# Optimization experiments

Hardware: AMD Instinct MI355X
Metric: run time of the kernel (lower is better)

The kernel has to match this reference:

```python
import math
import jax, jax.numpy as jnp
import numpy as np

B, T, H, E, K, F = 4, 4096, 512, 8, 2, 2048
CAP_FACTOR, ROUND_TO = 0.3125, 128


def _capacity(num_tokens):
    cap = math.ceil(CAP_FACTOR * num_tokens)
    cap = ROUND_TO * math.ceil(cap / ROUND_TO)
    return max(1, min(cap, num_tokens))


def setup_inputs() -> dict:
    key = jax.random.key(0)
    k0, k1, k2, k3 = jax.random.split(key, 4)
    x = jax.random.normal(k0, (B, T, H), jnp.float32)
    router_w = jax.random.normal(k1, (H, E), jnp.float32) * 0.02
    w1 = jax.random.normal(k2, (E, H, F), jnp.float32) * (1.0 / np.sqrt(H))
    b1 = jnp.zeros((E, F), jnp.float32)
    w2 = jax.random.normal(k3, (E, F, H), jnp.float32) * (1.0 / np.sqrt(F))
    b2 = jnp.zeros((E, H), jnp.float32)
    return {"x": x, "router_w": router_w, "w1": w1, "b1": b1, "w2": w2, "b2": b2}


def reference(x, router_w, w1, b1, w2, b2):
    Bc, Tc, Hc = x.shape
    n = Bc * Tc
    cap = _capacity(n)  # static: 5120
    flat = x.reshape(n, Hc)

    # Router + top-k selection (fp32 logits, softmax over selected logits)
    logits = (flat @ router_w).astype(jnp.float32)          # [n, E]
    sel_logits, expert_idx = jax.lax.top_k(logits, K)       # [n, K]
    weights = jax.nn.softmax(sel_logits, axis=-1)           # [n, K]

    # Flatten (token, k) assignments and sort by expert (stable)
    fe = expert_idx.reshape(-1).astype(jnp.int32)           # [n*K]
    fw = weights.reshape(-1)
    tok = jnp.broadcast_to(jnp.arange(n, dtype=jnp.int32)[:, None], expert_idx.shape).reshape(-1)
    order = jnp.argsort(fe)  # jax sort is stable
    se, st, sw = fe[order], tok[order], fw[order]

    # Per-expert slot index; assignments beyond capacity are dropped
    counts = jnp.bincount(se, length=E)                     # [E]
    offsets = (jnp.cumsum(counts) - counts).astype(jnp.int32)
    slot = jnp.arange(se.shape[0], dtype=jnp.int32) - offsets[se]
    keep = slot < cap
    sw = jnp.where(keep, sw, 0.0)                           # dropped tokens contribute 0

    # Pack into fixed-capacity expert buffers (out-of-range slots dropped)
    sx = flat[st]                                           # [n*K, H]
    expert_inputs = jnp.zeros((E, cap, Hc), flat.dtype).at[se, slot].set(sx, mode='drop')

    # Grouped expert MLP: Dense(F) -> GELU -> Dense(H)
    h = jax.nn.gelu(jnp.einsum('ech,ehf->ecf', expert_inputs, w1) + b1[:, None, :])
    out = jnp.einsum('ecf,efh->ech', h, w2) + b2[:, None, :]

    # Zero invalid (unused) slots
    clipped = jnp.minimum(counts, cap)
    valid = (jnp.arange(cap, dtype=jnp.int32)[None, :] < clipped[:, None])[..., None]
    out = jnp.where(valid, out, 0)

    # Scatter-combine weighted expert outputs back to tokens
    slot_c = jnp.minimum(slot, cap - 1)                     # dropped rows have weight 0
    gathered = out[se, slot_c] * sw[:, None].astype(out.dtype)
    combined = jnp.zeros((n, Hc), out.dtype).at[st].add(gathered)
    return combined.reshape(Bc, Tc, Hc)
```

## Files before the change

kernel.cpp:

```cpp
#include <hip/hip_runtime.h>
#include <hip/hip_bf16.h>

#define NTOK 16384
#define HD   512
#define ED   8
#define FD   2048
#define CAP  5120
#define NA   32768

typedef __bf16 bf16x8 __attribute__((ext_vector_type(8)));
typedef float  f32x4  __attribute__((ext_vector_type(4)));

static constexpr size_t OFF_EIDX = 0;
static constexpr size_t OFF_WGT  = 131072;
static constexpr size_t OFF_STOK = 262144;
static constexpr size_t OFF_SWGT = 458752;
static constexpr size_t OFF_W2T  = 1u << 20;
static constexpr size_t OFF_H    = OFF_W2T + (size_t)ED*HD*FD*2;
static constexpr size_t OFF_W1T  = OFF_H   + (size_t)ED*CAP*FD*2;
static constexpr size_t OFF_XBF  = OFF_W1T + (size_t)ED*FD*HD*2;

__device__ __forceinline__ unsigned short f2bf(float f) {
    __bf16 b = (__bf16)f;
    return __builtin_bit_cast(unsigned short, b);
}

__device__ __forceinline__ float gelu_fast(float v) {
    const float u = 1.5957691216057308f * (v + 0.044715f * v * v * v);
    return v / (1.f + __expf(-u));
}

__global__ __launch_bounds__(256) void transpose_cast_kernel(
    const float* __restrict__ in, unsigned short* __restrict__ out, int R, int C)
{
    __shared__ unsigned short tile[32][33];
    const int e = blockIdx.z;
    in  += (size_t)e * R * C;
    out += (size_t)e * R * C;
    const int r0 = blockIdx.y * 32, c0 = blockIdx.x * 32;
    const int tr = threadIdx.x >> 3, tc = (threadIdx.x & 7) * 4;
    const float4 v = *(const float4*)(in + (size_t)(r0 + tr) * C + c0 + tc);
    tile[tr][tc + 0] = f2bf(v.x);
    tile[tr][tc + 1] = f2bf(v.y);
    tile[tr][tc + 2] = f2bf(v.z);
    tile[tr][tc + 3] = f2bf(v.w);
    __syncthreads();
    ushort4 o;
    o.x = tile[tc + 0][tr]; o.y = tile[tc + 1][tr];
    o.z = tile[tc + 2][tr]; o.w = tile[tc + 3][tr];
    *(ushort4*)(out + (size_t)(c0 + tr) * R + r0 + tc) = o;
}

__global__ __launch_bounds__(256) void router_kernel(
    const float* __restrict__ x, const float* __restrict__ rw,
    int* __restrict__ eidx, float* __restrict__ wgt,
    unsigned short* __restrict__ xbf)
{
    __shared__ float rws[HD * ED];
    const int tid = threadIdx.x;
    for (int i = tid * 4; i < HD * ED; i += 256 * 4)
        *(float4*)(rws + i) = *(const float4*)(rw + i);
    __syncthreads();

    const int wid = tid >> 6, lane = tid & 63;
    const int t = blockIdx.x * 4 + wid;
    const float* xr = x + (size_t)t * HD;

    float acc[ED];
#pragma unroll
    for (int e = 0; e < ED; e++) acc[e] = 0.f;

    float4 xv0 = *(const float4*)(xr + lane * 8);
    float4 xv1 = *(const float4*)(xr + lane * 8 + 4);
    float xv[8] = {xv0.x, xv0.y, xv0.z, xv0.w, xv1.x, xv1.y, xv1.z, xv1.w};

    union { unsigned short us[8]; uint4 v; } pk;
#pragma unroll
    for (int j = 0; j < 8; j++) pk.us[j] = f2bf(xv[j]);
    *(uint4*)(xbf + (size_t)t * HD + lane * 8) = pk.v;

#pragma unroll
    for (int j = 0; j < 8; j++) {
        const int h = lane * 8 + j;
#pragma unroll
        for (int e = 0; e < ED; e++) acc[e] += xv[j] * rws[h * ED + e];
    }
#pragma unroll
    for (int off = 32; off >= 1; off >>= 1) {
#pragma unroll
        for (int e = 0; e < ED; e++) acc[e] += __shfl_down(acc[e], off);
    }
    if (lane == 0) {
        int e0 = 0; float l0 = acc[0];
        for (int e = 1; e < ED; e++) if (acc[e] > l0) { l0 = acc[e]; e0 = e; }
        int e1 = 0; float l1 = -1e30f;
        for (int e = 0; e < ED; e++) {
            if (e == e0) continue;
            if (acc[e] > l1) { l1 = acc[e]; e1 = e; }
        }
        const float ex = expf(l1 - l0);
        const float inv = 1.f / (1.f + ex);
        eidx[t * 2 + 0] = e0;  eidx[t * 2 + 1] = e1;
        wgt [t * 2 + 0] = inv; wgt [t * 2 + 1] = ex * inv;
    }
}

__global__ __launch_bounds__(1024) void scan_kernel(
    const int* __restrict__ eidx, const float* __restrict__ wgt,
    int* __restrict__ stok, float* __restrict__ swgt)
{
    __shared__ int running[ED];
    __shared__ int wcnt[16][ED];
    const int tid = threadIdx.x;

    for (int i = tid; i < ED * CAP; i += 1024) stok[i] = -1;
    if (tid < ED) running[tid] = 0;
    __syncthreads();

    const int lane = tid & 63, wid = tid >> 6;
    const unsigned long long below = (1ull << lane) - 1ull;

    for (int c = 0; c < NA / 1024; c++) {
        const int a = c * 1024 + tid;
        const int e = eidx[a];
        const float w = wgt[a];
        int myrank = 0;
#pragma unroll
        for (int ee = 0; ee < ED; ee++) {
            unsigned long long m = __ballot(e == ee);
            if (ee == e) myrank = __popcll(m & below);
            if (lane == 0) wcnt[wid][ee] = __popcll(m);
        }
        __syncthreads();
        int woff = 0;
        for (int ww = 0; ww < wid; ww++) woff += wcnt[ww][e];
        const int slot = running[e] + woff + myrank;
        if (slot < CAP) {
            stok[e * CAP + slot] = a >> 1;
            swgt[e * CAP + slot] = w;
        }
        __syncthreads();
        if (tid < ED) {
            int tot = 0;
            for (int ww = 0; ww < 16; ww++) tot += wcnt[ww][tid];
            running[tid] += tot;
        }
        __syncthreads();
    }
}

template<int KD, int ND, int NT, bool FUSE>
__global__ __launch_bounds__(256) void gemm_mfma(
    const unsigned short* __restrict__ Abase,
    const unsigned short* __restrict__ Bt,
    const float* __restrict__ bias,
    const int* __restrict__ stok,
    const float* __restrict__ swgt,
    unsigned short* __restrict__ hout,
    float* __restrict__ out)
{
    constexpr int RS   = 40;
    constexpr int BUFE = 128 * RS;
    __shared__ __align__(16) unsigned short As[2 * BUFE];
    __shared__ __align__(16) unsigned short Bs[2 * BUFE];

    const int tid = threadIdx.x;
    const int e  = blockIdx.x & 7;
    const int g  = blockIdx.x >> 3;
    const int n0 = (g % NT) * 128;
    const int m0 = (g / NT) * 128;

    const int q  = tid & 3;
    const int r1 = tid >> 2;
    const int r2 = r1 + 64;

    size_t ai1, ai2;
    if (!FUSE) {
        const int t1 = stok[e * CAP + m0 + r1];
        const int t2 = stok[e * CAP + m0 + r2];
        ai1 = (size_t)(t1 >= 0 ? t1 : 0);
        ai2 = (size_t)(t2 >= 0 ? t2 : 0);
    } else {
        ai1 = (size_t)(e * CAP + m0 + r1);
        ai2 = (size_t)(e * CAP + m0 + r2);
    }
    const unsigned short* arow1 = Abase + ai1 * KD + q * 8;
    const unsigned short* arow2 = Abase + ai2 * KD + q * 8;
    const unsigned short* brow1 = Bt + ((size_t)e * ND + n0 + r1) * KD + q * 8;
    const unsigned short* brow2 = Bt + ((size_t)e * ND + n0 + r2) * KD + q * 8;

    const int oW1 = r1 * RS + q * 8;
    const int oW2 = r2 * RS + q * 8;

    const int lane = tid & 63;
    const int wid  = tid >> 6;
    const int wrow = (wid & 1) * 64;
    const int wcol = (wid >> 1) * 64;
    const int l15  = lane & 15;
    const int quad = lane >> 4;
    const int fA   = (wrow + l15) * RS + quad * 8;
    const int fB   = (wcol + l15) * RS + quad * 8;

    f32x4 acc[4][4];
#pragma unroll
    for (int i = 0; i < 4; i++)
#pragma unroll
        for (int j = 0; j < 4; j++) acc[i][j] = (f32x4)0.f;

    float4 ra1 = *(const float4*)(arow1);
    float4 ra2 = *(const float4*)(arow2);
    float4 rb1 = *(const float4*)(brow1);
    float4 rb2 = *(const float4*)(brow2);
    *(float4*)(&As[oW1]) = ra1;
    *(float4*)(&As[oW2]) = ra2;
    *(float4*)(&Bs[oW1]) = rb1;
    *(float4*)(&Bs[oW2]) = rb2;
    if (32 < KD) {
        ra1 = *(const float4*)(arow1 + 32);
        ra2 = *(const float4*)(arow2 + 32);
        rb1 = *(const float4*)(brow1 + 32);
        rb2 = *(const float4*)(brow2 + 32);
    }
    __syncthreads();

#define COMPUTE(PBUF)                                                          \
    {                                                                          \
        const unsigned short* Ab = As + (PBUF) * BUFE;                         \
        const unsigned short* Bb = Bs + (PBUF) * BUFE;                         \
        bf16x8 af[4], bfv[4];                                                  \
        _Pragma("unroll")                                                      \
        for (int i = 0; i < 4; i++) af[i]  = *(const bf16x8*)(Ab + fA + i * 16 * RS); \
        _Pragma("unroll")                                                      \
        for (int j = 0; j < 4; j++) bfv[j] = *(const bf16x8*)(Bb + fB + j * 16 * RS); \
        _Pragma("unroll")                                                      \
        for (int i = 0; i < 4; i++)                                            \
            _Pragma("unroll")                                                  \
            for (int j = 0; j < 4; j++)                                        \
                acc[i][j] = __builtin_amdgcn_mfma_f32_16x16x32_bf16(           \
                    af[i], bfv[j], acc[i][j], 0, 0, 0);                        \
    }

    int rbuf = 0;
    for (int kc = 0; kc < KD; kc += 32) {
        const int wb = (rbuf ^ 1) * BUFE;
        if (kc + 32 < KD) {
            *(float4*)(&As[wb + oW1]) = ra1;
            *(float4*)(&As[wb + oW2]) = ra2;
            *(float4*)(&Bs[wb + oW1]) = rb1;
            *(float4*)(&Bs[wb + oW2]) = rb2;
            if (kc + 64 < KD) {
                ra1 = *(const float4*)(arow1 + kc + 64);
                ra2 = *(const float4*)(arow2 + kc + 64);
                rb1 = *(const float4*)(brow1 + kc + 64);
                rb2 = *(const float4*)(brow2 + kc + 64);
            }
        }
        COMPUTE(rbuf);
        __syncthreads();
        rbuf ^= 1;
    }
#undef COMPUTE

    if (!FUSE) {
#pragma unroll
        for (int i = 0; i < 4; i++) {
#pragma unroll
            for (int g2 = 0; g2 < 4; g2++) {
                const int m = wrow + i * 16 + quad * 4 + g2;
                unsigned short* hrow = hout + ((size_t)e * CAP + m0 + m) * FD + n0;
#pragma unroll
                for (int j = 0; j < 4; j++) {
                    const int n = wcol + j * 16 + l15;
                    const float v = acc[i][j][g2] + bias[(size_t)e * ND + n0 + n];
                    hrow[n] = f2bf(gelu_fast(v));
                }
            }
        }
    } else {
#pragma unroll
        for (int i = 0; i < 4; i++) {
#pragma unroll
            for (int g2 = 0; g2 < 4; g2++) {
                const int m = wrow + i * 16 + quad * 4 + g2;
                const int tok = stok[e * CAP + m0 + m];
                if (tok >= 0) {
                    const float w = swgt[e * CAP + m0 + m];
                    float* orow = out + (size_t)tok * HD + n0;
#pragma unroll
                    for (int j = 0; j < 4; j++) {
                        const int n = wcol + j * 16 + l15;
                        const float v = (acc[i][j][g2] + bias[(size_t)e * ND + n0 + n]) * w;
                        atomicAdd(orow + n, v);
                    }
                }
            }
        }
    }
}

extern "C" void kernel_launch(void* const* d_in, const int* in_sizes, int n_in,
                              void* d_out, int out_size, void* d_ws, size_t ws_size,
                              hipStream_t stream)
{
    const float* x  = (const float*)d_in[0];
    const float* rw = (const float*)d_in[1];
    const float* w1 = (const float*)d_in[2];
    const float* b1 = (const float*)d_in[3];
    const float* w2 = (const float*)d_in[4];
    const float* b2 = (const float*)d_in[5];
    float* out = (float*)d_out;

    char* ws = (char*)d_ws;
    int*   eidx = (int*)  (ws + OFF_EIDX);
    float* wgt  = (float*)(ws + OFF_WGT);
    int*   stok = (int*)  (ws + OFF_STOK);
    float* swgt = (float*)(ws + OFF_SWGT);
    unsigned short* w2t  = (unsigned short*)(ws + OFF_W2T);
    unsigned short* hbuf = (unsigned short*)(ws + OFF_H);
    unsigned short* w1t  = (unsigned short*)(ws + OFF_W1T);
    unsigned short* xbf  = (unsigned short*)(ws + OFF_XBF);

    transpose_cast_kernel<<<dim3(FD / 32, HD / 32, ED), 256, 0, stream>>>(w1, w1t, HD, FD);
    transpose_cast_kernel<<<dim3(HD / 32, FD / 32, ED), 256, 0, stream>>>(w2, w2t, FD, HD);
    router_kernel<<<NTOK / 4, 256, 0, stream>>>(x, rw, eidx, wgt, xbf);
    scan_kernel<<<1, 1024, 0, stream>>>(eidx, wgt, stok, swgt);
    hipMemsetAsync(d_out, 0, (size_t)out_size * sizeof(float), stream);

    gemm_mfma<HD, FD, FD/128, false>
        <<<8 * (FD/128) * (CAP/128), 256, 0, stream>>>(
        xbf, w1t, b1, stok, nullptr, hbuf, nullptr);

    gemm_mfma<FD, HD, HD/128, true>
        <<<8 * (HD/128) * (CAP/128), 256, 0, stream>>>(
        hbuf, w2t, b2, stok, swgt, nullptr, out);
}
```

Baseline: 521.5 us.

## Restructure scan into two-pass prefix, fuse output zeroing, reorganize GEMM LDS layout

Three independent changes. The output zeroing moves from a separate memset into the router kernel. The single-block scan is rewritten to count all chunks first, build the per-warp offsets in one serial pass, then scatter without per-chunk barriers. The GEMM shared-memory tiles switch from a padded row-major layout (stride 40) to a k-quad-major layout of 16-byte vectors, so fragment loads index contiguous vectors, which changes the LDS bank access pattern.

```diff
diff --git a/kernel.cpp b/kernel.cpp
--- a/kernel.cpp
+++ b/kernel.cpp
@@ -54,7 +54,7 @@
 __global__ __launch_bounds__(256) void router_kernel(
     const float* __restrict__ x, const float* __restrict__ rw,
     int* __restrict__ eidx, float* __restrict__ wgt,
-    unsigned short* __restrict__ xbf)
+    unsigned short* __restrict__ xbf, float* __restrict__ outz)
 {
     __shared__ float rws[HD * ED];
     const int tid = threadIdx.x;
@@ -65,6 +65,10 @@
     const int wid = tid >> 6, lane = tid & 63;
     const int t = blockIdx.x * 4 + wid;
     const float* xr = x + (size_t)t * HD;
+
+    const float4 z = make_float4(0.f, 0.f, 0.f, 0.f);
+    *(float4*)(outz + (size_t)t * HD + lane * 8)     = z;
+    *(float4*)(outz + (size_t)t * HD + lane * 8 + 4) = z;
 
     float acc[ED];
 #pragma unroll
@@ -109,43 +113,48 @@
     const int* __restrict__ eidx, const float* __restrict__ wgt,
     int* __restrict__ stok, float* __restrict__ swgt)
 {
-    __shared__ int running[ED];
-    __shared__ int wcnt[16][ED];
+    __shared__ int wcnt[32][16][ED];
     const int tid = threadIdx.x;
-
-    for (int i = tid; i < ED * CAP; i += 1024) stok[i] = -1;
-    if (tid < ED) running[tid] = 0;
-    __syncthreads();
-
     const int lane = tid & 63, wid = tid >> 6;
     const unsigned long long below = (1ull << lane) - 1ull;
+
+    for (int i = tid; i < ED * CAP; i += 1024) stok[i] = -1;
+
+    for (int c = 0; c < NA / 1024; c++) {
+        const int e = eidx[c * 1024 + tid];
+#pragma unroll
+        for (int ee = 0; ee < ED; ee++) {
+            unsigned long long m = __ballot(e == ee);
+            if (lane == 0) wcnt[c][wid][ee] = __popcll(m);
+        }
+    }
+    __syncthreads();
+
+    if (tid < ED) {
+        int run = 0;
+        for (int c = 0; c < 32; c++)
+            for (int w = 0; w < 16; w++) {
+                const int v = wcnt[c][w][tid];
+                wcnt[c][w][tid] = run;
+                run += v;
+            }
+    }
+    __syncthreads();
 
     for (int c = 0; c < NA / 1024; c++) {
         const int a = c * 1024 + tid;
         const int e = eidx[a];
-        const float w = wgt[a];
         int myrank = 0;
 #pragma unroll
         for (int ee = 0; ee < ED; ee++) {
             unsigned long long m = __ballot(e == ee);
             if (ee == e) myrank = __popcll(m & below);
-            if (lane == 0) wcnt[wid][ee] = __popcll(m);
-        }
-        __syncthreads();
-        int woff = 0;
-        for (int ww = 0; ww < wid; ww++) woff += wcnt[ww][e];
-        const int slot = running[e] + woff + myrank;
+        }
+        const int slot = wcnt[c][wid][e] + myrank;
         if (slot < CAP) {
             stok[e * CAP + slot] = a >> 1;
-            swgt[e * CAP + slot] = w;
-        }
-        __syncthreads();
-        if (tid < ED) {
-            int tot = 0;
-            for (int ww = 0; ww < 16; ww++) tot += wcnt[ww][tid];
-            running[tid] += tot;
-        }
-        __syncthreads();
+            swgt[e * CAP + slot] = wgt[a];
+        }
     }
 }
 
@@ -159,8 +168,7 @@
     unsigned short* __restrict__ hout,
     float* __restrict__ out)
 {
-    constexpr int RS   = 40;
-    constexpr int BUFE = 128 * RS;
+    constexpr int BUFE = 4096;
     __shared__ __align__(16) unsigned short As[2 * BUFE];
     __shared__ __align__(16) unsigned short Bs[2 * BUFE];
 
@@ -189,8 +197,8 @@
     const unsigned short* brow1 = Bt + ((size_t)e * ND + n0 + r1) * KD + q * 8;
     const unsigned short* brow2 = Bt + ((size_t)e * ND + n0 + r2) * KD + q * 8;
 
-    const int oW1 = r1 * RS + q * 8;
-    const int oW2 = r2 * RS + q * 8;
+    const int oW1 = (q * 128 + r1) * 8;
+    const int oW2 = (q * 128 + r2) * 8;
 
     const int lane = tid & 63;
     const int wid  = tid >> 6;
@@ -198,8 +206,7 @@
     const int wcol = (wid >> 1) * 64;
     const int l15  = lane & 15;
     const int quad = lane >> 4;
-    const int fA   = (wrow + l15) * RS + quad * 8;
-    const int fB   = (wcol + l15) * RS + quad * 8;
+    const int foff = quad * 128 + l15;
 
     f32x4 acc[4][4];
 #pragma unroll
@@ -225,13 +232,13 @@
 
 #define COMPUTE(PBUF)                                                          \
     {                                                                          \
-        const unsigned short* Ab = As + (PBUF) * BUFE;                         \
-        const unsigned short* Bb = Bs + (PBUF) * BUFE;                         \
+        const bf16x8* Av = (const bf16x8*)(As + (PBUF) * BUFE);                \
+        const bf16x8* Bv = (const bf16x8*)(Bs + (PBUF) * BUFE);                \
         bf16x8 af[4], bfv[4];                                                  \
         _Pragma("unroll")                                                      \
-        for (int i = 0; i < 4; i++) af[i]  = *(const bf16x8*)(Ab + fA + i * 16 * RS); \
+        for (int i = 0; i < 4; i++) af[i]  = Av[foff + wrow + i * 16];         \
         _Pragma("unroll")                                                      \
-        for (int j = 0; j < 4; j++) bfv[j] = *(const bf16x8*)(Bb + fB + j * 16 * RS); \
+        for (int j = 0; j < 4; j++) bfv[j] = Bv[foff + wcol + j * 16];         \
         _Pragma("unroll")                                                      \
         for (int i = 0; i < 4; i++)                                            \
             _Pragma("unroll")                                                  \
@@ -322,9 +329,8 @@
 
     transpose_cast_kernel<<<dim3(FD / 32, HD / 32, ED), 256, 0, stream>>>(w1, w1t, HD, FD);
     transpose_cast_kernel<<<dim3(HD / 32, FD / 32, ED), 256, 0, stream>>>(w2, w2t, FD, HD);
-    router_kernel<<<NTOK / 4, 256, 0, stream>>>(x, rw, eidx, wgt, xbf);
+    router_kernel<<<NTOK / 4, 256, 0, stream>>>(x, rw, eidx, wgt, xbf, out);
     scan_kernel<<<1, 1024, 0, stream>>>(eidx, wgt, stok, swgt);
-    hipMemsetAsync(d_out, 0, (size_t)out_size * sizeof(float), stream);
 
     gemm_mfma<HD, FD, FD/128, false>
         <<<8 * (FD/128) * (CAP/128), 256, 0, stream>>>(
```

Measured after the change: 534.1 us. 2.4% more time.
